# Performance work log

Hardware: AMD Instinct MI355X
Metric: run time of the kernel (lower is better)

The kernel has to match this reference:

```python
import jax, jax.numpy as jnp
import numpy as np

F = 512    # x_features
M = 8      # mid_features
C = 20     # classnum
B = 2048   # batch
MF = M * F

def _lin(k, fin, fout):
    k1, k2 = jax.random.split(k)
    s = 1.0 / np.sqrt(fin)
    W = jax.random.uniform(k1, (fout, fin), minval=-s, maxval=s, dtype=jnp.float32)
    b = jax.random.uniform(k2, (fout,), minval=-s, maxval=s, dtype=jnp.float32)
    return W, b

def setup_inputs():
    key = jax.random.key(0)
    ks = jax.random.split(key, 12)
    W1, b1 = _lin(ks[0], F, F)
    W2, b2 = _lin(ks[1], F, F)
    W3, b3 = _lin(ks[2], F, MF)
    W4, b4 = _lin(ks[3], F, MF)
    W5, b5 = _lin(ks[4], MF, C)
    W7, b7 = _lin(ks[5], MF, MF)
    W8, b8 = _lin(ks[6], MF, MF)
    W9, b9 = _lin(ks[7], MF, MF)
    x = jax.random.normal(ks[8], (B, F), dtype=jnp.float32)
    batch_label = jax.random.randint(ks[9], (B,), 0, C, dtype=jnp.int32)
    hs_init = jax.random.uniform(ks[10], (C, MF), dtype=jnp.float32)
    labels_init = jnp.zeros((C, MF), dtype=jnp.float32)
    return dict(x=x, batch_label=batch_label, W1=W1, b1=b1, W2=W2, b2=b2,
                W3=W3, b3=b3, W4=W4, b4=b4, W5=W5, b5=b5, W7=W7, b7=b7,
                W8=W8, b8=b8, W9=W9, b9=b9, hs_init=hs_init, labels_init=labels_init)

def reference(x, batch_label, W1, b1, W2, b2, W3, b3, W4, b4, W5, b5,
              W7, b7, W8, b8, W9, b9, hs_init, labels_init):
    h = jax.nn.relu(x @ W1.T + b1)
    h = jax.nn.relu(h @ W2.T + b2)
    label0 = jnp.tanh(h @ W3.T + b3)   # [B, MF]  (self.label_0)
    out = jnp.tanh(h @ W4.T + b4)      # [B, MF]
    gram = label0 @ label0.T           # [B, B]
    masks = batch_label[None, :] == jnp.arange(C, dtype=batch_label.dtype)[:, None]  # [C, B]
    counts = masks.sum(axis=1)         # [C]

    def attn_for_class(mask):
        # masked self-attention restricted to rows/cols of this class
        logits = jnp.where(mask[None, :], gram, -1e30)
        A = jax.nn.softmax(logits, axis=1)           # [B, B]
        attn = A @ label0                            # [B, MF]
        return jnp.sum(attn * mask[:, None].astype(attn.dtype), axis=0) / jnp.maximum(mask.sum(), 1)

    attn_labels = jax.vmap(attn_for_class)(masks)    # [C, MF]
    hs_new = jax.nn.sigmoid(attn_labels @ W7.T + b7 + hs_init @ W8.T + b8)
    hs_new = jax.lax.stop_gradient(hs_new)           # matches hs[i].detach_()
    nonempty = (counts > 0)[:, None]
    hs = jnp.where(nonempty, hs_new, hs_init)
    labels = jnp.where(nonempty, jnp.tanh(hs @ W9.T + b9), labels_init)  # [C, MF]
    # cosine similarity (torch eps = 1e-8)
    denom = jnp.maximum(jnp.linalg.norm(out, axis=1)[:, None] *
                        jnp.linalg.norm(labels, axis=1)[None, :], 1e-8)
    outs = (out @ labels.T) / denom                  # [B, C]  == outs.transpose(1,0)
    ls = jnp.tanh(labels @ W5.T + b5)                # [C, C]
    return jnp.concatenate([outs, ls], axis=0)       # [B+C, C]
```

## Files before the change

### kernel.cpp

```cpp
#include <hip/hip_runtime.h>
#include <hip/hip_bf16.h>
#include <math.h>

#define FDIM 512
#define MFD  4096
#define CNUM 20
#define BATCH 2048
#define SMAX 256
#define GKS  16
#define GBK  64

typedef __attribute__((ext_vector_type(8))) short bf16x8;
typedef __attribute__((ext_vector_type(4))) float f32x4;

__device__ inline unsigned short f2bf1(float f) {
  union { float f; unsigned u; } a; a.f = f;
  unsigned r = a.u + 0x7fffu + ((a.u >> 16) & 1u);
  return (unsigned short)(r >> 16);
}
__device__ inline float bf2f(unsigned short u) {
  union { unsigned u; float f; } a; a.u = ((unsigned)u) << 16; return a.f;
}
__device__ inline float fast_tanh(float x) {
  float cx = fminf(fmaxf(x, -15.f), 15.f);
  float e = __expf(2.f * cx);
  return (e - 1.f) / (e + 1.f);
}
__device__ inline float dot4acc(float4 a, float4 b, float acc) {
  acc = fmaf(a.x, b.x, acc); acc = fmaf(a.y, b.y, acc);
  acc = fmaf(a.z, b.z, acc); acc = fmaf(a.w, b.w, acc);
  return acc;
}
__device__ inline void gload_lds16(const void* g, void* l) {
  __builtin_amdgcn_global_load_lds(
      (const __attribute__((address_space(1))) unsigned int*)g,
      (__attribute__((address_space(3))) unsigned int*)l, 16, 0, 0);
}

__global__ __launch_bounds__(256) void cvt_bf16(const float* __restrict__ in,
                                                unsigned short* __restrict__ out, int n4) {
  int i = blockIdx.x * 256 + threadIdx.x;
  if (i >= n4) return;
  float4 v = ((const float4*)in)[i];
  ((ushort4*)out)[i] = make_ushort4(f2bf1(v.x), f2bf1(v.y), f2bf1(v.z), f2bf1(v.w));
}

template<int ACT, int OUTBF>
__global__ __launch_bounds__(256) void mfma_gemm(const unsigned short* __restrict__ A,
                                                 const unsigned short* __restrict__ B,
                                                 const float* __restrict__ bias,
                                                 float* __restrict__ Cf,
                                                 unsigned short* __restrict__ Cb,
                                                 int M, int N, int K) {
  __shared__ __align__(16) char lds[16384];
  const int t = threadIdx.x, lane = t & 63, w = t >> 6;
  const int wr = w >> 1, wc = w & 1;
  const int m0 = blockIdx.y * 128, n0 = blockIdx.x * 128;

  f32x4 acc[4][4];
#pragma unroll
  for (int m = 0; m < 4; ++m)
#pragma unroll
    for (int n = 0; n < 4; ++n) acc[m][n] = (f32x4){0.f, 0.f, 0.f, 0.f};

  int rS[2], qS[2];
#pragma unroll
  for (int i = 0; i < 2; ++i) {
    int t16 = (w * 2 + i) * 64 + lane;
    rS[i] = t16 >> 2;
    qS[i] = (t16 & 3) ^ ((rS[i] >> 1) & 3);
  }

  for (int k0 = 0; k0 < K; k0 += 32) {
#pragma unroll
    for (int i = 0; i < 2; ++i) {
      gload_lds16(A + (size_t)(m0 + rS[i]) * K + k0 + qS[i] * 8,
                  lds + (w * 2 + i) * 1024);
      gload_lds16(B + (size_t)(n0 + rS[i]) * K + k0 + qS[i] * 8,
                  lds + 8192 + (w * 2 + i) * 1024);
    }
    __syncthreads();

    bf16x8 af[4], bfr[4];
    const int kq = lane >> 4, l15 = lane & 15;
#pragma unroll
    for (int m = 0; m < 4; ++m) {
      int ra = wr * 64 + m * 16 + l15;
      af[m] = *(const bf16x8*)(lds + ra * 64 + ((kq ^ ((ra >> 1) & 3)) << 4));
      int rb = wc * 64 + m * 16 + l15;
      bfr[m] = *(const bf16x8*)(lds + 8192 + rb * 64 + ((kq ^ ((rb >> 1) & 3)) << 4));
    }
#pragma unroll
    for (int m = 0; m < 4; ++m)
#pragma unroll
      for (int n = 0; n < 4; ++n)
        acc[m][n] = __builtin_amdgcn_mfma_f32_16x16x32_bf16(af[m], bfr[n], acc[m][n], 0, 0, 0);
    __syncthreads();
  }

#pragma unroll
  for (int n = 0; n < 4; ++n) {
    int col = n0 + wc * 64 + n * 16 + (lane & 15);
    float bv = bias[col];
#pragma unroll
    for (int m = 0; m < 4; ++m) {
      int rbase = m0 + wr * 64 + m * 16 + ((lane >> 4) << 2);
#pragma unroll
      for (int j = 0; j < 4; ++j) {
        float v = acc[m][n][j] + bv;
        if (ACT == 1) v = fmaxf(v, 0.f);
        if (ACT == 2) v = fast_tanh(v);
        if (OUTBF) Cb[(size_t)(rbase + j) * N + col] = f2bf1(v);
        else       Cf[(size_t)(rbase + j) * N + col] = v;
      }
    }
  }
}

__global__ void build_idx(const int* __restrict__ label, int* __restrict__ idx,
                          int* __restrict__ counts) {
  __shared__ int cnt[CNUM];
  int t = threadIdx.x;
  if (t < CNUM) cnt[t] = 0;
  __syncthreads();
  for (int b = t; b < BATCH; b += 256) {
    int c = label[b];
    int p = atomicAdd(&cnt[c], 1);
    idx[c * BATCH + p] = b;
  }
  __syncthreads();
  if (t < CNUM) counts[t] = cnt[t];
}

__global__ __launch_bounds__(256) void gram_mfma(const unsigned short* __restrict__ Gb,
                                                 const int* __restrict__ idx,
                                                 const int* __restrict__ counts,
                                                 float* __restrict__ S) {
  const int c = blockIdx.z, n = counts[c];
  const int tp = blockIdx.y, ti = tp >> 1, tj = tp & 1;
  const int i0 = ti * 128, j0 = tj * 128;
  if (i0 >= n || j0 >= n) return;
  const int* idc = idx + c * BATCH;
  __shared__ __align__(16) char lds[32768];
  const bool same = (ti == tj);
  char* ldsB = same ? lds : (lds + 16384);

  const int t = threadIdx.x, lane = t & 63, w = t >> 6;
  size_t offA[4], offB[4];
#pragma unroll
  for (int q = 0; q < 4; ++q) {
    int t16 = q * 256 + t;
    int r = t16 >> 3, p = t16 & 7;
    int ch = p ^ (r & 7);
    int ia = i0 + r, jb = j0 + r;
    offA[q] = (size_t)idc[ia < n ? ia : 0] * MFD + ch * 8;
    offB[q] = (size_t)idc[jb < n ? jb : 0] * MFD + ch * 8;
  }
  const int kbeg = blockIdx.x * (MFD / GKS);

  f32x4 acc[2][8];
#pragma unroll
  for (int fi = 0; fi < 2; ++fi)
#pragma unroll
    for (int fj = 0; fj < 8; ++fj) acc[fi][fj] = (f32x4){0.f, 0.f, 0.f, 0.f};

  const int l15 = lane & 15, kq = lane >> 4;
  for (int k0 = kbeg; k0 < kbeg + MFD / GKS; k0 += GBK) {
#pragma unroll
    for (int q = 0; q < 4; ++q) {
      gload_lds16(Gb + offA[q] + k0, lds + q * 4096 + w * 1024 + (lane << 4));
      if (!same)
        gload_lds16(Gb + offB[q] + k0, ldsB + q * 4096 + w * 1024 + (lane << 4));
    }
    __syncthreads();
#pragma unroll
    for (int kk = 0; kk < 2; ++kk) {
      bf16x8 a[2], b[8];
#pragma unroll
      for (int fi = 0; fi < 2; ++fi) {
        int r = w * 32 + fi * 16 + l15;
        int sl = (kk * 4 + kq) ^ (r & 7);
        a[fi] = *(const bf16x8*)(lds + r * 128 + sl * 16);
      }
#pragma unroll
      for (int fj = 0; fj < 8; ++fj) {
        int r = fj * 16 + l15;
        int sl = (kk * 4 + kq) ^ (r & 7);
        b[fj] = *(const bf16x8*)(ldsB + r * 128 + sl * 16);
      }
#pragma unroll
      for (int fi = 0; fi < 2; ++fi)
#pragma unroll
        for (int fj = 0; fj < 8; ++fj)
          acc[fi][fj] = __builtin_amdgcn_mfma_f32_16x16x32_bf16(a[fi], b[fj], acc[fi][fj], 0, 0, 0);
    }
    __syncthreads();
  }

  float* Sc = S + (size_t)c * SMAX * SMAX;
#pragma unroll
  for (int fi = 0; fi < 2; ++fi) {
    int ibase = i0 + w * 32 + fi * 16 + (lane >> 4) * 4;
#pragma unroll
    for (int fj = 0; fj < 8; ++fj) {
      int j = j0 + fj * 16 + l15;
#pragma unroll
      for (int jj = 0; jj < 4; ++jj)
        atomicAdd(&Sc[(size_t)(ibase + jj) * SMAX + j], acc[fi][fj][jj]);
    }
  }
}

__global__ __launch_bounds__(256) void softmax_w2(const float* __restrict__ S,
                                                  const int* __restrict__ counts,
                                                  float* __restrict__ W) {
  const int c = blockIdx.y;
  const int n = counts[c];
  __shared__ float wacc[4][SMAX];
  const int t = threadIdx.x, lane = t & 63, wid = t >> 6;
  for (int j = t; j < 4 * SMAX; j += 256) (&wacc[0][0])[j] = 0.f;
  __syncthreads();
  const float* Sc = S + (size_t)c * SMAX * SMAX;
  for (int i = blockIdx.x * 4 + wid; i < n; i += 32) {
    const float* row = Sc + (size_t)i * SMAX;
    float v[4];
    float m = -INFINITY;
#pragma unroll
    for (int q = 0; q < 4; ++q) {
      int j = lane + q * 64;
      v[q] = (j < n) ? row[j] : -INFINITY;
      m = fmaxf(m, v[q]);
    }
#pragma unroll
    for (int s = 32; s; s >>= 1) m = fmaxf(m, __shfl_xor(m, s));
    float e[4], sum = 0.f;
#pragma unroll
    for (int q = 0; q < 4; ++q) {
      int j = lane + q * 64;
      e[q] = (j < n) ? expf(v[q] - m) : 0.f;
      sum += e[q];
    }
#pragma unroll
    for (int s = 32; s; s >>= 1) sum += __shfl_xor(sum, s);
    float inv = 1.f / sum;
#pragma unroll
    for (int q = 0; q < 4; ++q) {
      int j = lane + q * 64;
      if (j < n) wacc[wid][j] += e[q] * inv;
    }
  }
  __syncthreads();
  for (int j = t; j < SMAX; j += 256) {
    float v = wacc[0][j] + wacc[1][j] + wacc[2][j] + wacc[3][j];
    if (v != 0.f) atomicAdd(&W[c * SMAX + j], v);
  }
}

__global__ __launch_bounds__(256) void attn_combine2(const unsigned short* __restrict__ Gb,
                                                     const int* __restrict__ idx,
                                                     const int* __restrict__ counts,
                                                     const float* __restrict__ W,
                                                     float* __restrict__ attn) {
  const int c = blockIdx.y, n = counts[c];
  const int col2 = blockIdx.x * 256 + threadIdx.x;
  const int* idc = idx + c * BATCH;
  const float* Wc = W + c * SMAX;
  float a0 = 0.f, a1 = 0.f;
#pragma unroll 4
  for (int j = 0; j < n; ++j) {
    float wj = Wc[j];
    ushort2 g = ((const ushort2*)(Gb + (size_t)idc[j] * MFD))[col2];
    a0 = fmaf(wj, bf2f(g.x), a0);
    a1 = fmaf(wj, bf2f(g.y), a1);
  }
  float inv = (n > 0) ? 1.f / (float)n : 0.f;
  ((float2*)attn)[(size_t)c * (MFD / 2) + col2] = make_float2(a0 * inv, a1 * inv);
}

__global__ __launch_bounds__(256) void skinny_hs(const float* __restrict__ attn,
                                                 const float* __restrict__ hsin,
                                                 const float* __restrict__ W7,
                                                 const float* __restrict__ b7,
                                                 const float* __restrict__ W8,
                                                 const float* __restrict__ b8,
                                                 const int* __restrict__ counts,
                                                 float* __restrict__ hs) {
  const int t = threadIdx.x, lane = t & 63, wid = t >> 6;
  const int o0 = blockIdx.x * 16 + wid * 4;
  const float4* A4 = (const float4*)attn;
  const float4* H4 = (const float4*)hsin;
  float acc[CNUM][4] = {};
  for (int i = 0; i < MFD / 4 / 64; ++i) {
    int k4 = lane + i * 64;
    float4 w7v[4], w8v[4];
#pragma unroll
    for (int o = 0; o < 4; ++o) {
      w7v[o] = *((const float4*)(W7 + (size_t)(o0 + o) * MFD) + k4);
      w8v[o] = *((const float4*)(W8 + (size_t)(o0 + o) * MFD) + k4);
    }
#pragma unroll
    for (int c = 0; c < CNUM; ++c) {
      float4 av = A4[(size_t)c * (MFD / 4) + k4];
      float4 hv = H4[(size_t)c * (MFD / 4) + k4];
#pragma unroll
      for (int o = 0; o < 4; ++o)
        acc[c][o] = dot4acc(hv, w8v[o], dot4acc(av, w7v[o], acc[c][o]));
    }
  }
#pragma unroll
  for (int c = 0; c < CNUM; ++c)
#pragma unroll
    for (int o = 0; o < 4; ++o)
#pragma unroll
      for (int s = 32; s; s >>= 1) acc[c][o] += __shfl_xor(acc[c][o], s);
  if (lane == 0) {
#pragma unroll
    for (int c = 0; c < CNUM; ++c) {
      bool ne = counts[c] > 0;
#pragma unroll
      for (int o = 0; o < 4; ++o) {
        int oo = o0 + o;
        float v = acc[c][o] + b7[oo] + b8[oo];
        v = 1.f / (1.f + expf(-v));
        hs[(size_t)c * MFD + oo] = ne ? v : hsin[(size_t)c * MFD + oo];
      }
    }
  }
}

__global__ __launch_bounds__(256) void skinny_lab(const float* __restrict__ hsv,
                                                  const float* __restrict__ W9,
                                                  const float* __restrict__ b9,
                                                  const int* __restrict__ counts,
                                                  const float* __restrict__ labinit,
                                                  float* __restrict__ labels) {
  const int t = threadIdx.x, lane = t & 63, wid = t >> 6;
  const int o0 = blockIdx.x * 16 + wid * 4;
  const float4* H4 = (const float4*)hsv;
  float acc[CNUM][4] = {};
  for (int i = 0; i < MFD / 4 / 64; ++i) {
    int k4 = lane + i * 64;
    float4 w9v[4];
#pragma unroll
    for (int o = 0; o < 4; ++o)
      w9v[o] = *((const float4*)(W9 + (size_t)(o0 + o) * MFD) + k4);
#pragma unroll
    for (int c = 0; c < CNUM; ++c) {
      float4 hv = H4[(size_t)c * (MFD / 4) + k4];
#pragma unroll
      for (int o = 0; o < 4; ++o) acc[c][o] = dot4acc(hv, w9v[o], acc[c][o]);
    }
  }
#pragma unroll
  for (int c = 0; c < CNUM; ++c)
#pragma unroll
    for (int o = 0; o < 4; ++o)
#pragma unroll
      for (int s = 32; s; s >>= 1) acc[c][o] += __shfl_xor(acc[c][o], s);
  if (lane == 0) {
#pragma unroll
    for (int c = 0; c < CNUM; ++c) {
      bool ne = counts[c] > 0;
#pragma unroll
      for (int o = 0; o < 4; ++o) {
        int oo = o0 + o;
        float v = tanhf(acc[c][o] + b9[oo]);
        labels[(size_t)c * MFD + oo] = ne ? v : labinit[(size_t)c * MFD + oo];
      }
    }
  }
}

__global__ __launch_bounds__(256) void rownorm(const float* __restrict__ X,
                                               float* __restrict__ out, int ncols) {
  const int b = blockIdx.x, t = threadIdx.x;
  const float4* X4 = (const float4*)(X + (size_t)b * ncols);
  float ss = 0.f;
  for (int i = t; i < ncols / 4; i += 256) {
    float4 v = X4[i];
    ss = dot4acc(v, v, ss);
  }
#pragma unroll
  for (int s = 32; s; s >>= 1) ss += __shfl_xor(ss, s);
  __shared__ float red[4];
  const int lane = t & 63, wid = t >> 6;
  if (lane == 0) red[wid] = ss;
  __syncthreads();
  if (t == 0) out[b] = sqrtf(red[0] + red[1] + red[2] + red[3]);
}

__global__ __launch_bounds__(256) void outs_kernel(const float* __restrict__ outb,
                                                   const float* __restrict__ labels,
                                                   const float* __restrict__ no,
                                                   const float* __restrict__ nl,
                                                   float* __restrict__ dout) {
  const int b = blockIdx.x, t = threadIdx.x;
  const float4* O4 = (const float4*)(outb + (size_t)b * MFD);
  const float4* L4 = (const float4*)labels;
  float acc[CNUM] = {};
  for (int i = t; i < MFD / 4; i += 256) {
    float4 ov = O4[i];
#pragma unroll
    for (int c = 0; c < CNUM; ++c)
      acc[c] = dot4acc(ov, L4[(size_t)c * (MFD / 4) + i], acc[c]);
  }
#pragma unroll
  for (int c = 0; c < CNUM; ++c)
#pragma unroll
    for (int s = 32; s; s >>= 1) acc[c] += __shfl_xor(acc[c], s);
  __shared__ float red[4][CNUM];
  const int lane = t & 63, wid = t >> 6;
  if (lane == 0) {
#pragma unroll
    for (int c = 0; c < CNUM; ++c) red[wid][c] = acc[c];
  }
  __syncthreads();
  if (t < CNUM) {
    float v = red[0][t] + red[1][t] + red[2][t] + red[3][t];
    float d = fmaxf(no[b] * nl[t], 1e-8f);
    dout[(size_t)b * CNUM + t] = v / d;
  }
}

__global__ __launch_bounds__(256) void ls_kernel(const float* __restrict__ labels,
                                                 const float* __restrict__ W5,
                                                 const float* __restrict__ b5,
                                                 float* __restrict__ dout) {
  const int c1 = blockIdx.x, t = threadIdx.x;
  __shared__ float lrow[MFD];
  for (int i = t; i < MFD; i += 256) lrow[i] = labels[(size_t)c1 * MFD + i];
  __syncthreads();
  const int lane = t & 63, wid = t >> 6;
  for (int c2 = wid; c2 < CNUM; c2 += 4) {
    const float4* w = (const float4*)(W5 + (size_t)c2 * MFD);
    float acc = 0.f;
    for (int i = lane; i < MFD / 4; i += 64)
      acc = dot4acc(*(const float4*)&lrow[i * 4], w[i], acc);
#pragma unroll
    for (int s = 32; s; s >>= 1) acc += __shfl_xor(acc, s);
    if (lane == 0)
      dout[(size_t)(BATCH + c1) * CNUM + c2] = tanhf(acc + b5[c2]);
  }
}

extern "C" void kernel_launch(void* const* d_in, const int* in_sizes, int n_in,
                              void* d_out, int out_size, void* d_ws, size_t ws_size,
                              hipStream_t stream) {
  const float* x    = (const float*)d_in[0];
  const int*   lab  = (const int*)d_in[1];
  const float* W1 = (const float*)d_in[2];  const float* b1 = (const float*)d_in[3];
  const float* W2 = (const float*)d_in[4];  const float* b2 = (const float*)d_in[5];
  const float* W3 = (const float*)d_in[6];  const float* b3 = (const float*)d_in[7];
  const float* W4 = (const float*)d_in[8];  const float* b4 = (const float*)d_in[9];
  const float* W5 = (const float*)d_in[10]; const float* b5 = (const float*)d_in[11];
  const float* W7 = (const float*)d_in[12]; const float* b7 = (const float*)d_in[13];
  const float* W8 = (const float*)d_in[14]; const float* b8 = (const float*)d_in[15];
  const float* W9 = (const float*)d_in[16]; const float* b9 = (const float*)d_in[17];
  const float* hs_init  = (const float*)d_in[18];
  const float* lab_init = (const float*)d_in[19];
  float* out = (float*)d_out;

  char* base = (char*)d_ws;
  size_t off = 0;
  auto alloc = [&](size_t bytes) { char* p = base + off; off += (bytes + 255) & ~(size_t)255; return p; };

  unsigned short* xb  = (unsigned short*)alloc((size_t)BATCH * FDIM * 2);
  unsigned short* h1b = (unsigned short*)alloc((size_t)BATCH * FDIM * 2);
  unsigned short* h2b = (unsigned short*)alloc((size_t)BATCH * FDIM * 2);
  unsigned short* W1b = (unsigned short*)alloc((size_t)FDIM * FDIM * 2);
  unsigned short* W2b = (unsigned short*)alloc((size_t)FDIM * FDIM * 2);
  unsigned short* W3b = (unsigned short*)alloc((size_t)MFD * FDIM * 2);
  unsigned short* W4b = (unsigned short*)alloc((size_t)MFD * FDIM * 2);
  unsigned short* label0b = (unsigned short*)alloc((size_t)BATCH * MFD * 2);
  float* outb   = (float*)alloc((size_t)BATCH * MFD * 4);
  float* S      = (float*)alloc((size_t)CNUM * SMAX * SMAX * 4);
  float* wsum   = (float*)alloc((size_t)CNUM * SMAX * 4);
  float* attn   = (float*)alloc((size_t)CNUM * MFD * 4);
  float* hsbuf  = (float*)alloc((size_t)CNUM * MFD * 4);
  float* labels = (float*)alloc((size_t)CNUM * MFD * 4);
  float* no     = (float*)alloc((size_t)BATCH * 4);
  float* nl     = (float*)alloc(64 * 4);
  int* idx      = (int*)alloc((size_t)CNUM * BATCH * 4);
  int* counts   = (int*)alloc(64 * 4);

  cvt_bf16<<<(BATCH * FDIM / 4 + 255) / 256, 256, 0, stream>>>(x,  xb,  BATCH * FDIM / 4);
  cvt_bf16<<<(FDIM * FDIM / 4 + 255) / 256, 256, 0, stream>>>(W1, W1b, FDIM * FDIM / 4);
  cvt_bf16<<<(FDIM * FDIM / 4 + 255) / 256, 256, 0, stream>>>(W2, W2b, FDIM * FDIM / 4);
  cvt_bf16<<<(MFD * FDIM / 4 + 255) / 256, 256, 0, stream>>>(W3, W3b, MFD * FDIM / 4);
  cvt_bf16<<<(MFD * FDIM / 4 + 255) / 256, 256, 0, stream>>>(W4, W4b, MFD * FDIM / 4);

  mfma_gemm<1, 1><<<dim3(FDIM / 128, BATCH / 128), 256, 0, stream>>>(xb,  W1b, b1, nullptr, h1b, BATCH, FDIM, FDIM);
  mfma_gemm<1, 1><<<dim3(FDIM / 128, BATCH / 128), 256, 0, stream>>>(h1b, W2b, b2, nullptr, h2b, BATCH, FDIM, FDIM);
  mfma_gemm<2, 1><<<dim3(MFD / 128, BATCH / 128), 256, 0, stream>>>(h2b, W3b, b3, nullptr, label0b, BATCH, MFD, FDIM);
  mfma_gemm<2, 0><<<dim3(MFD / 128, BATCH / 128), 256, 0, stream>>>(h2b, W4b, b4, outb,   nullptr,  BATCH, MFD, FDIM);

  build_idx<<<1, 256, 0, stream>>>(lab, idx, counts);
  hipMemsetAsync(S, 0, (size_t)CNUM * SMAX * SMAX * 4 + (size_t)CNUM * SMAX * 4, stream);
  gram_mfma<<<dim3(GKS, 4, CNUM), 256, 0, stream>>>(label0b, idx, counts, S);
  softmax_w2<<<dim3(8, CNUM), 256, 0, stream>>>(S, counts, wsum);
  attn_combine2<<<dim3(MFD / 512, CNUM), 256, 0, stream>>>(label0b, idx, counts, wsum, attn);
  skinny_hs<<<MFD / 16, 256, 0, stream>>>(attn, hs_init, W7, b7, W8, b8, counts, hsbuf);
  skinny_lab<<<MFD / 16, 256, 0, stream>>>(hsbuf, W9, b9, counts, lab_init, labels);
  rownorm<<<BATCH, 256, 0, stream>>>(outb, no, MFD);
  rownorm<<<CNUM, 256, 0, stream>>>(labels, nl, MFD);
  outs_kernel<<<BATCH, 256, 0, stream>>>(outb, labels, no, nl, out);
  ls_kernel<<<CNUM, 256, 0, stream>>>(labels, W5, b5, out);
}
```

Measured before the change: 601.2 us.

## Split-K skinny GEMMs and attn combine with atomics, fuse row norm into outs

The attention combine kernel is split along the member dimension into four chunks that accumulate into attn with atomics. The W7/W8 and W9 skinny matrix-vector kernels are restructured into split-K accumulation kernels (one output row per wave, four K slices) that write partial sums atomically, followed by small finalize kernels for the bias, activation and empty-class selection. The separate row-norm pass over outb is folded into the outs kernel. The aim is more parallelism in the small kernels and one fewer read of the large out buffer, at the cost of extra memsets, atomics and launches.

```diff
diff --git a/kernel.cpp b/kernel.cpp
--- a/kernel.cpp
+++ b/kernel.cpp
@@ -9,6 +9,8 @@
 #define SMAX 256
 #define GKS  16
 #define GBK  64
+#define SKS  4
+#define AJS  4
 
 typedef __attribute__((ext_vector_type(8))) short bf16x8;
 typedef __attribute__((ext_vector_type(4))) float f32x4;
@@ -256,118 +258,93 @@
   }
 }
 
-__global__ __launch_bounds__(256) void attn_combine2(const unsigned short* __restrict__ Gb,
+__global__ __launch_bounds__(256) void attn_combine3(const unsigned short* __restrict__ Gb,
                                                      const int* __restrict__ idx,
                                                      const int* __restrict__ counts,
                                                      const float* __restrict__ W,
                                                      float* __restrict__ attn) {
-  const int c = blockIdx.y, n = counts[c];
+  const int c = blockIdx.z, n = counts[c];
   const int col2 = blockIdx.x * 256 + threadIdx.x;
+  const int j0 = (n * (int)blockIdx.y) / AJS;
+  const int j1 = (n * ((int)blockIdx.y + 1)) / AJS;
   const int* idc = idx + c * BATCH;
   const float* Wc = W + c * SMAX;
   float a0 = 0.f, a1 = 0.f;
-#pragma unroll 4
-  for (int j = 0; j < n; ++j) {
+  for (int j = j0; j < j1; ++j) {
     float wj = Wc[j];
     ushort2 g = ((const ushort2*)(Gb + (size_t)idc[j] * MFD))[col2];
     a0 = fmaf(wj, bf2f(g.x), a0);
     a1 = fmaf(wj, bf2f(g.y), a1);
   }
-  float inv = (n > 0) ? 1.f / (float)n : 0.f;
-  ((float2*)attn)[(size_t)c * (MFD / 2) + col2] = make_float2(a0 * inv, a1 * inv);
-}
-
-__global__ __launch_bounds__(256) void skinny_hs(const float* __restrict__ attn,
-                                                 const float* __restrict__ hsin,
-                                                 const float* __restrict__ W7,
-                                                 const float* __restrict__ b7,
-                                                 const float* __restrict__ W8,
-                                                 const float* __restrict__ b8,
-                                                 const int* __restrict__ counts,
-                                                 float* __restrict__ hs) {
+  if (j1 > j0) {
+    float inv = 1.f / (float)n;
+    atomicAdd(&attn[(size_t)c * MFD + col2 * 2],     a0 * inv);
+    atomicAdd(&attn[(size_t)c * MFD + col2 * 2 + 1], a1 * inv);
+  }
+}
+
+template<int TWO>
+__global__ __launch_bounds__(256) void skinny_acc(const float* __restrict__ Wa,
+                                                  const float* __restrict__ Aa,
+                                                  const float* __restrict__ Wb,
+                                                  const float* __restrict__ Ab,
+                                                  float* __restrict__ accbuf) {
   const int t = threadIdx.x, lane = t & 63, wid = t >> 6;
-  const int o0 = blockIdx.x * 16 + wid * 4;
-  const float4* A4 = (const float4*)attn;
-  const float4* H4 = (const float4*)hsin;
-  float acc[CNUM][4] = {};
-  for (int i = 0; i < MFD / 4 / 64; ++i) {
-    int k4 = lane + i * 64;
-    float4 w7v[4], w8v[4];
-#pragma unroll
-    for (int o = 0; o < 4; ++o) {
-      w7v[o] = *((const float4*)(W7 + (size_t)(o0 + o) * MFD) + k4);
-      w8v[o] = *((const float4*)(W8 + (size_t)(o0 + o) * MFD) + k4);
-    }
+  const int o = blockIdx.x * 4 + wid;
+  const int kb4 = blockIdx.y * (MFD / 4 / SKS);
+  const float4* W4a = (const float4*)Wa + (size_t)o * (MFD / 4) + kb4;
+  const float4* W4b = (const float4*)Wb + (size_t)o * (MFD / 4) + kb4;
+  const float4* A4a = (const float4*)Aa + kb4;
+  const float4* A4b = (const float4*)Ab + kb4;
+  float acc[CNUM] = {};
+#pragma unroll
+  for (int i = 0; i < MFD / 4 / SKS / 64; ++i) {
+    int k4 = i * 64 + lane;
+    float4 wv = W4a[k4];
+    float4 wv2;
+    if (TWO) wv2 = W4b[k4];
 #pragma unroll
     for (int c = 0; c < CNUM; ++c) {
-      float4 av = A4[(size_t)c * (MFD / 4) + k4];
-      float4 hv = H4[(size_t)c * (MFD / 4) + k4];
-#pragma unroll
-      for (int o = 0; o < 4; ++o)
-        acc[c][o] = dot4acc(hv, w8v[o], dot4acc(av, w7v[o], acc[c][o]));
+      acc[c] = dot4acc(A4a[(size_t)c * (MFD / 4) + k4], wv, acc[c]);
+      if (TWO) acc[c] = dot4acc(A4b[(size_t)c * (MFD / 4) + k4], wv2, acc[c]);
     }
   }
 #pragma unroll
   for (int c = 0; c < CNUM; ++c)
 #pragma unroll
-    for (int o = 0; o < 4; ++o)
-#pragma unroll
-      for (int s = 32; s; s >>= 1) acc[c][o] += __shfl_xor(acc[c][o], s);
-  if (lane == 0) {
-#pragma unroll
-    for (int c = 0; c < CNUM; ++c) {
-      bool ne = counts[c] > 0;
-#pragma unroll
-      for (int o = 0; o < 4; ++o) {
-        int oo = o0 + o;
-        float v = acc[c][o] + b7[oo] + b8[oo];
-        v = 1.f / (1.f + expf(-v));
-        hs[(size_t)c * MFD + oo] = ne ? v : hsin[(size_t)c * MFD + oo];
-      }
-    }
-  }
-}
-
-__global__ __launch_bounds__(256) void skinny_lab(const float* __restrict__ hsv,
-                                                  const float* __restrict__ W9,
-                                                  const float* __restrict__ b9,
-                                                  const int* __restrict__ counts,
-                                                  const float* __restrict__ labinit,
-                                                  float* __restrict__ labels) {
-  const int t = threadIdx.x, lane = t & 63, wid = t >> 6;
-  const int o0 = blockIdx.x * 16 + wid * 4;
-  const float4* H4 = (const float4*)hsv;
-  float acc[CNUM][4] = {};
-  for (int i = 0; i < MFD / 4 / 64; ++i) {
-    int k4 = lane + i * 64;
-    float4 w9v[4];
-#pragma unroll
-    for (int o = 0; o < 4; ++o)
-      w9v[o] = *((const float4*)(W9 + (size_t)(o0 + o) * MFD) + k4);
-#pragma unroll
-    for (int c = 0; c < CNUM; ++c) {
-      float4 hv = H4[(size_t)c * (MFD / 4) + k4];
-#pragma unroll
-      for (int o = 0; o < 4; ++o) acc[c][o] = dot4acc(hv, w9v[o], acc[c][o]);
-    }
-  }
+    for (int s = 32; s; s >>= 1) acc[c] += __shfl_xor(acc[c], s);
 #pragma unroll
   for (int c = 0; c < CNUM; ++c)
-#pragma unroll
-    for (int o = 0; o < 4; ++o)
-#pragma unroll
-      for (int s = 32; s; s >>= 1) acc[c][o] += __shfl_xor(acc[c][o], s);
-  if (lane == 0) {
-#pragma unroll
-    for (int c = 0; c < CNUM; ++c) {
-      bool ne = counts[c] > 0;
-#pragma unroll
-      for (int o = 0; o < 4; ++o) {
-        int oo = o0 + o;
-        float v = tanhf(acc[c][o] + b9[oo]);
-        labels[(size_t)c * MFD + oo] = ne ? v : labinit[(size_t)c * MFD + oo];
-      }
-    }
+    if (lane == c) atomicAdd(&accbuf[(size_t)o * CNUM + c], acc[c]);
+}
+
+__global__ __launch_bounds__(256) void finalize_hs(const float* __restrict__ accbuf,
+                                                   const float* __restrict__ b7,
+                                                   const float* __restrict__ b8,
+                                                   const int* __restrict__ counts,
+                                                   const float* __restrict__ hsin,
+                                                   float* __restrict__ hs) {
+  const int o = blockIdx.x * 256 + threadIdx.x;
+  const float bb = b7[o] + b8[o];
+#pragma unroll
+  for (int c = 0; c < CNUM; ++c) {
+    float v = accbuf[(size_t)o * CNUM + c] + bb;
+    v = 1.f / (1.f + __expf(-v));
+    hs[(size_t)c * MFD + o] = (counts[c] > 0) ? v : hsin[(size_t)c * MFD + o];
+  }
+}
+
+__global__ __launch_bounds__(256) void finalize_lab(const float* __restrict__ accbuf,
+                                                    const float* __restrict__ b9,
+                                                    const int* __restrict__ counts,
+                                                    const float* __restrict__ labinit,
+                                                    float* __restrict__ labels) {
+  const int o = blockIdx.x * 256 + threadIdx.x;
+  const float bb = b9[o];
+#pragma unroll
+  for (int c = 0; c < CNUM; ++c) {
+    float v = tanhf(accbuf[(size_t)o * CNUM + c] + bb);
+    labels[(size_t)c * MFD + o] = (counts[c] > 0) ? v : labinit[(size_t)c * MFD + o];
   }
 }
 
@@ -389,35 +366,40 @@
   if (t == 0) out[b] = sqrtf(red[0] + red[1] + red[2] + red[3]);
 }
 
-__global__ __launch_bounds__(256) void outs_kernel(const float* __restrict__ outb,
-                                                   const float* __restrict__ labels,
-                                                   const float* __restrict__ no,
-                                                   const float* __restrict__ nl,
-                                                   float* __restrict__ dout) {
+__global__ __launch_bounds__(256) void outs_fused(const float* __restrict__ outb,
+                                                  const float* __restrict__ labels,
+                                                  const float* __restrict__ nl,
+                                                  float* __restrict__ dout) {
   const int b = blockIdx.x, t = threadIdx.x;
   const float4* O4 = (const float4*)(outb + (size_t)b * MFD);
   const float4* L4 = (const float4*)labels;
   float acc[CNUM] = {};
+  float ss = 0.f;
   for (int i = t; i < MFD / 4; i += 256) {
     float4 ov = O4[i];
+    ss = dot4acc(ov, ov, ss);
 #pragma unroll
     for (int c = 0; c < CNUM; ++c)
       acc[c] = dot4acc(ov, L4[(size_t)c * (MFD / 4) + i], acc[c]);
   }
 #pragma unroll
+  for (int s = 32; s; s >>= 1) ss += __shfl_xor(ss, s);
+#pragma unroll
   for (int c = 0; c < CNUM; ++c)
 #pragma unroll
     for (int s = 32; s; s >>= 1) acc[c] += __shfl_xor(acc[c], s);
-  __shared__ float red[4][CNUM];
+  __shared__ float red[4][CNUM + 1];
   const int lane = t & 63, wid = t >> 6;
   if (lane == 0) {
 #pragma unroll
     for (int c = 0; c < CNUM; ++c) red[wid][c] = acc[c];
+    red[wid][CNUM] = ss;
   }
   __syncthreads();
   if (t < CNUM) {
     float v = red[0][t] + red[1][t] + red[2][t] + red[3][t];
-    float d = fmaxf(no[b] * nl[t], 1e-8f);
+    float nrm = sqrtf(red[0][CNUM] + red[1][CNUM] + red[2][CNUM] + red[3][CNUM]);
+    float d = fmaxf(nrm * nl[t], 1e-8f);
     dout[(size_t)b * CNUM + t] = v / d;
   }
 }
@@ -476,9 +458,10 @@
   float* S      = (float*)alloc((size_t)CNUM * SMAX * SMAX * 4);
   float* wsum   = (float*)alloc((size_t)CNUM * SMAX * 4);
   float* attn   = (float*)alloc((size_t)CNUM * MFD * 4);
+  float* accA   = (float*)alloc((size_t)MFD * CNUM * 4);
+  float* accB   = (float*)alloc((size_t)MFD * CNUM * 4);
   float* hsbuf  = (float*)alloc((size_t)CNUM * MFD * 4);
   float* labels = (float*)alloc((size_t)CNUM * MFD * 4);
-  float* no     = (float*)alloc((size_t)BATCH * 4);
   float* nl     = (float*)alloc(64 * 4);
   int* idx      = (int*)alloc((size_t)CNUM * BATCH * 4);
   int* counts   = (int*)alloc(64 * 4);
@@ -495,14 +478,18 @@
   mfma_gemm<2, 0><<<dim3(MFD / 128, BATCH / 128), 256, 0, stream>>>(h2b, W4b, b4, outb,   nullptr,  BATCH, MFD, FDIM);
 
   build_idx<<<1, 256, 0, stream>>>(lab, idx, counts);
-  hipMemsetAsync(S, 0, (size_t)CNUM * SMAX * SMAX * 4 + (size_t)CNUM * SMAX * 4, stream);
+  hipMemsetAsync(S, 0, (size_t)CNUM * SMAX * SMAX * 4 + (size_t)CNUM * SMAX * 4 + (size_t)CNUM * MFD * 4, stream);
+  hipMemsetAsync(accA, 0, (size_t)MFD * CNUM * 8, stream);
   gram_mfma<<<dim3(GKS, 4, CNUM), 256, 0, stream>>>(label0b, idx, counts, S);
   softmax_w2<<<dim3(8, CNUM), 256, 0, stream>>>(S, counts, wsum);
-  attn_combine2<<<dim3(MFD / 512, CNUM), 256, 0, stream>>>(label0b, idx, counts, wsum, attn);
-  skinny_hs<<<MFD / 16, 256, 0, stream>>>(attn, hs_init, W7, b7, W8, b8, counts, hsbuf);
-  skinny_lab<<<MFD / 16, 256, 0, stream>>>(hsbuf, W9, b9, counts, lab_init, labels);
-  rownorm<<<BATCH, 256, 0, stream>>>(outb, no, MFD);
+  attn_combine3<<<dim3(MFD / 512, AJS, CNUM), 256, 0, stream>>>(label0b, idx, counts, wsum, attn);
+
+  skinny_acc<1><<<dim3(MFD / 4, SKS), 256, 0, stream>>>(W7, attn, W8, hs_init, accA);
+  finalize_hs<<<MFD / 256, 256, 0, stream>>>(accA, b7, b8, counts, hs_init, hsbuf);
+  skinny_acc<0><<<dim3(MFD / 4, SKS), 256, 0, stream>>>(W9, hsbuf, nullptr, nullptr, accB);
+  finalize_lab<<<MFD / 256, 256, 0, stream>>>(accB, b9, counts, lab_init, labels);
+
   rownorm<<<CNUM, 256, 0, stream>>>(labels, nl, MFD);
-  outs_kernel<<<BATCH, 256, 0, stream>>>(outb, labels, no, nl, out);
+  outs_fused<<<BATCH, 256, 0, stream>>>(outb, labels, nl, out);
   ls_kernel<<<CNUM, 256, 0, stream>>>(labels, W5, b5, out);
 }
```

After: 627.3 us. 1.04x slower.
